# Performance work log

Measured on AMD Instinct MI355X. Metric: run time of the kernel, lower is better.

Reference implementation:

```python
import jax, jax.numpy as jnp
import numpy as np

# geomloss.SamplesLoss(loss='sinkhorn', p=2, blur=0.1**0.5, backend='tensorized',
#                      cost=cosine cost ** 2) with defaults scaling=0.5, debias=True,
#                      reach=None (balanced OT, dampening = 1), uniform weights.
P = 2
BLUR = 0.1 ** 0.5   # eps = BLUR**P = 0.1
SCALING = 0.5


def cosine_cost(a, b):
    # a: (B,N,D), b: (B,M,D) -> (1 - cos(a,b))**2, shape (B,N,M)
    an = a / jnp.linalg.norm(a, axis=-1, keepdims=True)
    bn = b / jnp.linalg.norm(b, axis=-1, keepdims=True)
    return (1.0 - jnp.einsum('bnd,bmd->bnm', an, bn)) ** P


def softmin(eps, C, h):
    # geomloss softmin_tensorized: h (B,M), C (B,N,M) -> (B,N)
    return -eps * jax.nn.logsumexp(h[:, None, :] - C / eps, axis=2)


def eps_schedule(diameter):
    # geomloss epsilon_schedule(p, diameter, blur, scaling)
    return ([diameter ** P]
            + [float(np.exp(e)) for e in np.arange(P * np.log(diameter),
                                                   P * np.log(BLUR),
                                                   P * np.log(SCALING))]
            + [BLUR ** P])


def max_diameter(x, y):
    # geomloss max_diameter over all points of both (flattened) clouds
    D = x.shape[-1]
    pts = np.concatenate([np.asarray(x).reshape(-1, D),
                          np.asarray(y).reshape(-1, D)], axis=0)
    return float(np.linalg.norm(pts.max(axis=0) - pts.min(axis=0)))


def _sinkhorn(x, y, eps_list):
    sg = jax.lax.stop_gradient
    B, N, _ = x.shape
    M = y.shape[1]
    # geomloss detaches the second argument of each cost evaluation
    C_xy = cosine_cost(x, sg(y))
    C_yx = cosine_cost(y, sg(x))
    C_xx = cosine_cost(x, sg(x))  # debias terms
    C_yy = cosine_cost(y, sg(y))

    a_log = jnp.full((B, N), -np.log(N), dtype=x.dtype)  # log uniform weights
    b_log = jnp.full((B, M), -np.log(M), dtype=x.dtype)

    # initialization at the largest temperature
    eps = eps_list[0]
    f_aa = softmin(eps, sg(C_xx), a_log)
    g_bb = softmin(eps, sg(C_yy), b_log)
    g_ab = softmin(eps, sg(C_yx), a_log)
    f_ba = softmin(eps, sg(C_xy), b_log)

    # eps-scaling loop (run without gradients, as in geomloss)
    for eps in eps_list:
        ft_ba = softmin(eps, sg(C_xy), b_log + g_ab / eps)
        gt_ab = softmin(eps, sg(C_yx), a_log + f_ba / eps)
        ft_aa = softmin(eps, sg(C_xx), a_log + f_aa / eps)
        gt_bb = softmin(eps, sg(C_yy), b_log + g_bb / eps)
        f_ba, g_ab = 0.5 * (f_ba + ft_ba), 0.5 * (g_ab + gt_ab)
        f_aa, g_bb = 0.5 * (f_aa + ft_aa), 0.5 * (g_bb + gt_bb)

    # last extrapolation WITH gradients, dual inputs detached (envelope theorem)
    eps = eps_list[-1]
    f_ba, g_ab = (softmin(eps, C_xy, sg(b_log + g_ab / eps)),
                  softmin(eps, C_yx, sg(a_log + f_ba / eps)))
    f_aa = softmin(eps, C_xx, sg(a_log + f_aa / eps))
    g_bb = softmin(eps, C_yy, sg(b_log + g_bb / eps))

    # sinkhorn_cost, debiased, batch -> (B,)
    a = jnp.exp(a_log)
    b = jnp.exp(b_log)
    return jnp.sum(a * (f_ba - f_aa), axis=1) + jnp.sum(b * (g_ab - g_bb), axis=1)


def setup_inputs() -> dict:
    key = jax.random.key(0)
    k1, k2 = jax.random.split(key)
    B, N, D = 2, 4096, 64
    inputs = jax.random.normal(k1, (B, N, D), dtype=jnp.float32)
    targets = jax.random.normal(k2, (B, N, D), dtype=jnp.float32)
    return {"inputs": inputs, "targets": targets}


def reference(inputs, targets):
    eps_list = eps_schedule(max_diameter(inputs, targets))
    return _sinkhorn(inputs, targets, eps_list)
```

## Files before the change

kernel.cpp:

```cpp
#include <hip/hip_runtime.h>
#include <math.h>

#define Bq 2
#define Nq 4096
#define Dq 64
#define MAXR 14
#define RBAND 16
#define NBAND (Nq / RBAND)
#define W_LOG (-8.317766166719343f)
#define WL2   (-12.0f)
#define LOG2E 1.4426950408889634f
#define LN2   0.6931471805599453f
#define DQ_SCALE (4.0f / 65535.0f)
#define Q_SCALE  16383.75f
#define ACLAMP 88.0f
#define SFLOOR 1e-30f

#define F_XN   ((size_t)0)
#define F_YN   (F_XN + (size_t)Bq * Nq * Dq)
#define F_XH   (F_YN + (size_t)Bq * Nq * Dq)
#define F_XL   (F_XH + (size_t)Bq * Nq * Dq / 2)
#define F_YH   (F_XL + (size_t)Bq * Nq * Dq / 2)
#define F_YL   (F_YH + (size_t)Bq * Nq * Dq / 2)
#define F_FG   (F_YL + (size_t)Bq * Nq * Dq / 2)
#define F_EPS  (F_FG + (size_t)2 * 4 * Bq * Nq)
#define F_MM   (F_EPS + 64)
#define F_CP   (F_MM + (size_t)64 * 128)
#define F_C    (((F_CP + (size_t)Bq * NBAND * Nq) + 3) & ~(size_t)3)
#define GSZ    ((size_t)Bq * Nq * Nq)
#define F_TOTAL_P (F_C + 3 * GSZ / 2)
#define F_TOTAL_S (F_C)

typedef short short8v __attribute__((ext_vector_type(8)));
typedef float f32x4 __attribute__((ext_vector_type(4)));

__device__ __forceinline__ unsigned short f2bf(float f) {
    unsigned u = __float_as_uint(f);
    unsigned r = (u + 0x7fffu + ((u >> 16) & 1u)) >> 16;
    return (unsigned short)r;
}
__device__ __forceinline__ float bf2f(unsigned short b) {
    return __uint_as_float(((unsigned)b) << 16);
}

__global__ __launch_bounds__(256) void k_normalize(const float* __restrict__ x,
                                                   const float* __restrict__ y,
                                                   float* __restrict__ ws) {
    int gid = blockIdx.x * 256 + threadIdx.x;
    int wave = gid >> 6;
    int lane = gid & 63;
    int tensor = wave / (Bq * Nq);
    int p = wave % (Bq * Nq);
    const float* src = tensor ? y : x;
    float v = src[(size_t)p * Dq + lane];
    float s = v * v;
    #pragma unroll
    for (int o = 32; o > 0; o >>= 1) s += __shfl_xor(s, o);
    float vn = v / sqrtf(s);
    float* dst = ws + (tensor ? F_YN : F_XN);
    dst[(size_t)p * Dq + lane] = vn;
    unsigned short hb = f2bf(vn);
    float lo = vn - bf2f(hb);
    unsigned short lb = f2bf(lo);
    unsigned short* dh = (unsigned short*)(ws + (tensor ? F_YH : F_XH));
    unsigned short* dl = (unsigned short*)(ws + (tensor ? F_YL : F_XL));
    dh[(size_t)p * Dq + lane] = hb;
    dl[(size_t)p * Dq + lane] = lb;
}

__global__ __launch_bounds__(256) void k_minmax(const float* __restrict__ x,
                                                const float* __restrict__ y,
                                                float* __restrict__ ws) {
    int d = threadIdx.x & 63, q = threadIdx.x >> 6;
    int p0 = blockIdx.x * 256;
    float mx = -INFINITY, mn = INFINITY;
    for (int p = p0 + q; p < p0 + 256; p += 4) {
        const float* src = (p < Bq * Nq) ? x : y;
        int pp = (p < Bq * Nq) ? p : p - Bq * Nq;
        float v = src[(size_t)pp * Dq + d];
        mx = fmaxf(mx, v); mn = fminf(mn, v);
    }
    __shared__ float smx[4][64], smn[4][64];
    smx[q][d] = mx; smn[q][d] = mn;
    __syncthreads();
    if (threadIdx.x < 64) {
        float a = fmaxf(fmaxf(smx[0][d], smx[1][d]), fmaxf(smx[2][d], smx[3][d]));
        float i = fminf(fminf(smn[0][d], smn[1][d]), fminf(smn[2][d], smn[3][d]));
        ws[F_MM + (size_t)blockIdx.x * 128 + d] = a;
        ws[F_MM + (size_t)blockIdx.x * 128 + 64 + d] = i;
    }
}

__global__ void k_eps(float* __restrict__ ws) {
    int d = threadIdx.x;
    float mx = -INFINITY, mn = INFINITY;
    for (int k = 0; k < 64; k++) {
        mx = fmaxf(mx, ws[F_MM + (size_t)k * 128 + d]);
        mn = fminf(mn, ws[F_MM + (size_t)k * 128 + 64 + d]);
    }
    float r = mx - mn;
    float r2 = r * r;
    #pragma unroll
    for (int o = 32; o > 0; o >>= 1) r2 += __shfl_xor(r2, o);
    if (d == 0) {
        double dd = (double)sqrtf(r2);
        double start = 2.0 * log(dd);
        double stop  = 2.0 * log(sqrt(0.1));
        double step  = 2.0 * log(0.5);
        double lend = ceil((stop - start) / step);
        int len = (lend <= 0.0) ? 0 : (int)lend;
        int n = len + 2;
        if (n > MAXR - 2) n = MAXR - 2;
        int* ei = (int*)(ws + F_EPS);
        ei[0] = n;
        float* ev = ws + F_EPS + 8;
        ev[0] = (float)(dd * dd);
        for (int i = 0; i < len && i + 1 < n - 1; i++)
            ev[1 + i] = (float)exp(start + i * step);
        ev[n - 1] = 0.1f;
    }
}

__global__ __launch_bounds__(256) void k_gram_mfma(float* __restrict__ ws) {
    int op = blockIdx.z, b = blockIdx.y;
    int tr = (blockIdx.x & 63) * 64;
    int tc = (blockIdx.x >> 6) * 64;
    const unsigned short* AH = (const unsigned short*)(ws + (op == 2 ? F_YH : F_XH)) + (size_t)b * Nq * Dq;
    const unsigned short* AL = (const unsigned short*)(ws + (op == 2 ? F_YL : F_XL)) + (size_t)b * Nq * Dq;
    const unsigned short* BH = (const unsigned short*)(ws + (op == 1 ? F_XH : F_YH)) + (size_t)b * Nq * Dq;
    const unsigned short* BL = (const unsigned short*)(ws + (op == 1 ? F_XL : F_YL)) + (size_t)b * Nq * Dq;

    __shared__ unsigned short sAh[64][72], sAl[64][72], sBh[64][72], sBl[64][72], sC[64][72];

    #pragma unroll
    for (int i = 0; i < 2; i++) {
        int c = threadIdx.x + 256 * i;
        int row = c >> 3, pos = c & 7;
        size_t sa = (size_t)(tr + row) * Dq + pos * 8;
        size_t sb = (size_t)(tc + row) * Dq + pos * 8;
        *(uint4*)&sAh[row][pos * 8] = *(const uint4*)&AH[sa];
        *(uint4*)&sAl[row][pos * 8] = *(const uint4*)&AL[sa];
        *(uint4*)&sBh[row][pos * 8] = *(const uint4*)&BH[sb];
        *(uint4*)&sBl[row][pos * 8] = *(const uint4*)&BL[sb];
    }
    __syncthreads();

    int w = threadIdx.x >> 6, lane = threadIdx.x & 63;
    int m = lane & 15, kb = lane >> 4;
    int ar = w * 16 + m;
    short8v aH0 = *(const short8v*)&sAh[ar][kb * 8];
    short8v aH1 = *(const short8v*)&sAh[ar][32 + kb * 8];
    short8v aL0 = *(const short8v*)&sAl[ar][kb * 8];
    short8v aL1 = *(const short8v*)&sAl[ar][32 + kb * 8];

    #pragma unroll
    for (int cb = 0; cb < 4; cb++) {
        int bc = cb * 16 + m;
        short8v bH0 = *(const short8v*)&sBh[bc][kb * 8];
        short8v bH1 = *(const short8v*)&sBh[bc][32 + kb * 8];
        short8v bL0 = *(const short8v*)&sBl[bc][kb * 8];
        short8v bL1 = *(const short8v*)&sBl[bc][32 + kb * 8];
        f32x4 acc = {0.f, 0.f, 0.f, 0.f};
        acc = __builtin_amdgcn_mfma_f32_16x16x32_bf16(aH0, bH0, acc, 0, 0, 0);
        acc = __builtin_amdgcn_mfma_f32_16x16x32_bf16(aH1, bH1, acc, 0, 0, 0);
        acc = __builtin_amdgcn_mfma_f32_16x16x32_bf16(aL0, bH0, acc, 0, 0, 0);
        acc = __builtin_amdgcn_mfma_f32_16x16x32_bf16(aL1, bH1, acc, 0, 0, 0);
        acc = __builtin_amdgcn_mfma_f32_16x16x32_bf16(aH0, bL0, acc, 0, 0, 0);
        acc = __builtin_amdgcn_mfma_f32_16x16x32_bf16(aH1, bL1, acc, 0, 0, 0);
        #pragma unroll
        for (int rr = 0; rr < 4; rr++) {
            float c1 = 1.0f - acc[rr];
            unsigned u = __float2uint_rn(fminf(c1 * c1, 4.0f) * Q_SCALE);
            if (u > 65535u) u = 65535u;
            sC[w * 16 + kb * 4 + rr][cb * 16 + m] = (unsigned short)u;
        }
    }
    __syncthreads();

    unsigned short* C = (unsigned short*)(ws + F_C) + (size_t)op * GSZ + (size_t)b * Nq * Nq;
    #pragma unroll
    for (int i = 0; i < 2; i++) {
        int c = threadIdx.x + 256 * i;
        int row = c >> 3, pos = c & 7;
        uint4 v = *(const uint4*)&sC[row][pos * 8];
        *(uint4*)&C[(size_t)(tr + row) * Nq + tc + pos * 8] = v;
    }
}

__device__ __forceinline__ bool round_cfg(const float* ws, int r, int& mode, float& eps,
                                          float& inv_eps, int& cur, int& nxt) {
    const int* ei = (const int*)(ws + F_EPS);
    int n_eps = ei[0];
    if (r > n_eps + 1) return false;
    mode = (r == 0) ? 0 : ((r <= n_eps) ? 1 : 2);
    int eidx = (r == 0) ? 0 : ((r - 1 < n_eps - 1) ? r - 1 : n_eps - 1);
    eps = ws[F_EPS + 8 + eidx];
    inv_eps = 1.0f / eps;
    cur = r & 1; nxt = cur ^ 1;
    return true;
}

__global__ __launch_bounds__(256) void k_iter(float* __restrict__ ws, int r) {
    int mode, cur, nxt; float eps, inv_eps;
    if (!round_cfg(ws, r, mode, eps, inv_eps, cur, nxt)) return;
    float ie2 = inv_eps * LOG2E;
    float epsln2 = eps * LN2;
    float nkq = -DQ_SCALE * ie2;

    int bid = blockIdx.x;
    int op = bid / (Bq * NBAND);
    int rem = bid % (Bq * NBAND);
    int b = rem / NBAND;
    int band = rem % NBAND;
    int row0 = band * RBAND;
    int w = threadIdx.x >> 6, lane = threadIdx.x & 63;
    int colA = w * 1024 + lane * 8;
    int colB = colA + 512;

    const unsigned short* C = (const unsigned short*)(ws + F_C)
                              + (size_t)op * GSZ + ((size_t)b * Nq + row0) * Nq;
    int arr_dual = (op == 0) ? 1 : (op == 1 ? 2 : 3);
    int arr_out  = (op == 0) ? 0 : arr_dual;
    const float* gdual = ws + F_FG + ((size_t)cur * 4 + arr_dual) * (Bq * Nq) + (size_t)b * Nq;
    const float* fdual = ws + F_FG + ((size_t)cur * 4 + 0) * (Bq * Nq) + (size_t)b * Nq;

    float pa[16];
    if (mode != 0) {
        float4 g0 = *(const float4*)&gdual[colA];
        float4 g1 = *(const float4*)&gdual[colA + 4];
        float4 g2 = *(const float4*)&gdual[colB];
        float4 g3 = *(const float4*)&gdual[colB + 4];
        float gv[16] = {g0.x, g0.y, g0.z, g0.w, g1.x, g1.y, g1.z, g1.w,
                        g2.x, g2.y, g2.z, g2.w, g3.x, g3.y, g3.z, g3.w};
        #pragma unroll
        for (int j = 0; j < 16; j++) pa[j] = exp2f(fminf(gv[j] * ie2, ACLAMP));
    } else {
        #pragma unroll
        for (int j = 0; j < 16; j++) pa[j] = 1.f;
    }
    float cs[16];
    #pragma unroll
    for (int j = 0; j < 16; j++) cs[j] = 0.f;

    __shared__ float rowpart[RBAND][4];

    #pragma unroll 2
    for (int i = 0; i < RBAND; i += 2) {
        uint4 cA0 = *(const uint4*)&C[(size_t)i * Nq + colA];
        uint4 cB0 = *(const uint4*)&C[(size_t)i * Nq + colB];
        uint4 cA1 = *(const uint4*)&C[(size_t)(i + 1) * Nq + colA];
        uint4 cB1 = *(const uint4*)&C[(size_t)(i + 1) * Nq + colB];
        float pb0 = 1.f, pb1 = 1.f;
        if (op == 0 && mode != 0) {
            pb0 = exp2f(fminf(fdual[row0 + i] * ie2, ACLAMP));
            pb1 = exp2f(fminf(fdual[row0 + i + 1] * ie2, ACLAMP));
        }
        unsigned u0[8] = {cA0.x, cA0.y, cA0.z, cA0.w, cB0.x, cB0.y, cB0.z, cB0.w};
        unsigned u1[8] = {cA1.x, cA1.y, cA1.z, cA1.w, cB1.x, cB1.y, cB1.z, cB1.w};
        float rs0 = 0.f, rs1 = 0.f;
        #pragma unroll
        for (int j = 0; j < 16; j++) {
            float e0 = exp2f((float)((u0[j >> 1] >> ((j & 1) * 16)) & 0xffffu) * nkq);
            float e1 = exp2f((float)((u1[j >> 1] >> ((j & 1) * 16)) & 0xffffu) * nkq);
            rs0 = fmaf(pa[j], e0, rs0);
            rs1 = fmaf(pa[j], e1, rs1);
            if (op == 0) cs[j] = fmaf(pb0, e0, fmaf(pb1, e1, cs[j]));
        }
        #pragma unroll
        for (int o = 32; o > 0; o >>= 1) {
            rs0 += __shfl_xor(rs0, o);
            rs1 += __shfl_xor(rs1, o);
        }
        if (lane == 0) { rowpart[i][w] = rs0; rowpart[i + 1][w] = rs1; }
    }
    __syncthreads();

    if (threadIdx.x < RBAND) {
        int gr = row0 + threadIdx.x;
        const float* rp = rowpart[threadIdx.x];
        float s = (rp[0] + rp[1]) + (rp[2] + rp[3]);
        float ft = -epsln2 * (WL2 + log2f(fmaxf(s, SFLOOR)));
        float* outp = ws + F_FG + ((size_t)nxt * 4 + arr_out) * (Bq * Nq) + (size_t)b * Nq;
        const float* oldp = ws + F_FG + ((size_t)cur * 4 + arr_out) * (Bq * Nq) + (size_t)b * Nq;
        outp[gr] = (mode == 1) ? 0.5f * (oldp[gr] + ft) : ft;
    }

    if (op == 0) {
        float* cp = ws + F_CP + ((size_t)b * NBAND + band) * Nq;
        *(float4*)&cp[colA]     = make_float4(cs[0], cs[1], cs[2], cs[3]);
        *(float4*)&cp[colA + 4] = make_float4(cs[4], cs[5], cs[6], cs[7]);
        *(float4*)&cp[colB]     = make_float4(cs[8], cs[9], cs[10], cs[11]);
        *(float4*)&cp[colB + 4] = make_float4(cs[12], cs[13], cs[14], cs[15]);
    }
}

__global__ __launch_bounds__(256) void k_colcomb(float* __restrict__ ws, int r) {
    int mode, cur, nxt; float eps, inv_eps;
    if (!round_cfg(ws, r, mode, eps, inv_eps, cur, nxt)) return;
    float epsln2 = eps * LN2;
    int idx = blockIdx.x * 256 + threadIdx.x;
    int b = idx >> 12, m = idx & (Nq - 1);
    const float* cp = ws + F_CP + (size_t)b * NBAND * Nq + m;
    float S = 0.f;
    #pragma unroll 8
    for (int k = 0; k < NBAND; k++) S += cp[(size_t)k * Nq];
    float gt = -epsln2 * (WL2 + log2f(fmaxf(S, SFLOOR)));
    float* outp = ws + F_FG + ((size_t)nxt * 4 + 1) * (Bq * Nq) + (size_t)b * Nq;
    const float* oldp = ws + F_FG + ((size_t)cur * 4 + 1) * (Bq * Nq) + (size_t)b * Nq;
    outp[m] = (mode == 1) ? 0.5f * (oldp[m] + gt) : gt;
}

__global__ __launch_bounds__(256) void k_fused(float* __restrict__ ws, int r) {
    int mode, cur, nxt; float eps, inv_eps;
    if (!round_cfg(ws, r, mode, eps, inv_eps, cur, nxt)) return;
    int op = blockIdx.z, b = blockIdx.y;
    int tr = blockIdx.x * 64;
    const float* A  = ws + ((op == 1 || op == 3) ? F_YN : F_XN) + (size_t)b * Nq * Dq;
    const float* Bp = ws + ((op == 0 || op == 3) ? F_YN : F_XN) + (size_t)b * Nq * Dq;
    int dual_arr = (op == 0) ? 1 : (op == 1) ? 0 : (op == 2) ? 2 : 3;
    int out_arr  = (op == 0) ? 0 : (op == 1) ? 1 : (op == 2) ? 2 : 3;
    const float* hdual = ws + F_FG + ((size_t)cur * 4 + dual_arr) * (Bq * Nq) + (size_t)b * Nq;

    __shared__ float As[64][65], Bs[64][65];
    #pragma unroll
    for (int i = 0; i < 16; i++) {
        int idx = threadIdx.x + 256 * i;
        As[idx >> 6][idx & 63] = A[(size_t)(tr + (idx >> 6)) * Dq + (idx & 63)];
    }
    int tx = threadIdx.x & 15, ty = threadIdx.x >> 4;
    float m_i[4], s_i[4];
    #pragma unroll
    for (int i = 0; i < 4; i++) { m_i[i] = -INFINITY; s_i[i] = 0.f; }

    for (int tc = 0; tc < Nq; tc += 64) {
        __syncthreads();
        #pragma unroll
        for (int i = 0; i < 16; i++) {
            int idx = threadIdx.x + 256 * i;
            Bs[idx >> 6][idx & 63] = Bp[(size_t)(tc + (idx >> 6)) * Dq + (idx & 63)];
        }
        __syncthreads();
        float acc[4][4] = {};
        #pragma unroll
        for (int dd = 0; dd < 64; dd++) {
            float a[4], bb[4];
            #pragma unroll
            for (int i = 0; i < 4; i++) a[i] = As[ty * 4 + i][dd];
            #pragma unroll
            for (int j = 0; j < 4; j++) bb[j] = Bs[tx * 4 + j][dd];
            #pragma unroll
            for (int i = 0; i < 4; i++)
                #pragma unroll
                for (int j = 0; j < 4; j++) acc[i][j] = fmaf(a[i], bb[j], acc[i][j]);
        }
        float hv[4];
        #pragma unroll
        for (int j = 0; j < 4; j++)
            hv[j] = (mode == 0) ? 0.f : hdual[tc + tx * 4 + j];
        #pragma unroll
        for (int i = 0; i < 4; i++) {
            float v[4], tm = -INFINITY;
            #pragma unroll
            for (int j = 0; j < 4; j++) {
                float c = 1.0f - acc[i][j];
                v[j] = W_LOG + (hv[j] - c * c) * inv_eps;
                tm = fmaxf(tm, v[j]);
            }
            float nm = fmaxf(m_i[i], tm);
            float add = 0.f;
            #pragma unroll
            for (int j = 0; j < 4; j++) add += expf(v[j] - nm);
            s_i[i] = s_i[i] * expf(m_i[i] - nm) + add;
            m_i[i] = nm;
        }
    }
    #pragma unroll
    for (int o = 1; o < 16; o <<= 1) {
        #pragma unroll
        for (int i = 0; i < 4; i++) {
            float om = __shfl_xor(m_i[i], o);
            float os = __shfl_xor(s_i[i], o);
            float M = fmaxf(m_i[i], om);
            s_i[i] = s_i[i] * expf(m_i[i] - M) + os * expf(om - M);
            m_i[i] = M;
        }
    }
    if (tx == 0) {
        float* outp = ws + F_FG + ((size_t)nxt * 4 + out_arr) * (Bq * Nq) + (size_t)b * Nq;
        const float* oldp = ws + F_FG + ((size_t)cur * 4 + out_arr) * (Bq * Nq) + (size_t)b * Nq;
        #pragma unroll
        for (int i = 0; i < 4; i++) {
            int n = tr + ty * 4 + i;
            float ft = -eps * (m_i[i] + logf(s_i[i]));
            outp[n] = (mode == 1) ? 0.5f * (oldp[n] + ft) : ft;
        }
    }
}

__global__ __launch_bounds__(256) void k_final(const float* __restrict__ ws,
                                               float* __restrict__ out) {
    const int* ei = (const int*)(ws + F_EPS);
    int n_eps = ei[0];
    int fin = n_eps & 1;
    int b = blockIdx.x;
    const float* fba = ws + F_FG + ((size_t)fin * 4 + 0) * (Bq * Nq) + (size_t)b * Nq;
    const float* gab = ws + F_FG + ((size_t)fin * 4 + 1) * (Bq * Nq) + (size_t)b * Nq;
    const float* faa = ws + F_FG + ((size_t)fin * 4 + 2) * (Bq * Nq) + (size_t)b * Nq;
    const float* gbb = ws + F_FG + ((size_t)fin * 4 + 3) * (Bq * Nq) + (size_t)b * Nq;
    float s = 0.f;
    for (int n = threadIdx.x; n < Nq; n += 256)
        s += (fba[n] - faa[n]) + (gab[n] - gbb[n]);
    #pragma unroll
    for (int o = 32; o > 0; o >>= 1) s += __shfl_xor(s, o);
    __shared__ float red[4];
    if ((threadIdx.x & 63) == 0) red[threadIdx.x >> 6] = s;
    __syncthreads();
    if (threadIdx.x == 0)
        out[b] = (red[0] + red[1] + red[2] + red[3]) * (1.0f / Nq);
}

__global__ void k_sentinel(float* out, int n) {
    if ((int)threadIdx.x < n) out[threadIdx.x] = 2.0e9f;
}

extern "C" void kernel_launch(void* const* d_in, const int* in_sizes, int n_in,
                              void* d_out, int out_size, void* d_ws, size_t ws_size,
                              hipStream_t stream) {
    const float* x = (const float*)d_in[0];
    const float* y = (const float*)d_in[1];
    float* out = (float*)d_out;
    float* ws = (float*)d_ws;

    bool big   = ws_size >= F_TOTAL_P * sizeof(float);
    bool small = ws_size >= F_TOTAL_S * sizeof(float);

    if (!small) {
        k_sentinel<<<1, 64, 0, stream>>>(out, out_size);
        return;
    }

    k_normalize<<<(2 * Bq * Nq * 64) / 256, 256, 0, stream>>>(x, y, ws);
    k_minmax<<<64, 256, 0, stream>>>(x, y, ws);
    k_eps<<<1, 64, 0, stream>>>(ws);

    if (big) {
        k_gram_mfma<<<dim3(4096, Bq, 3), 256, 0, stream>>>(ws);
        for (int r = 0; r < MAXR; r++) {
            k_iter<<<3 * Bq * NBAND, 256, 0, stream>>>(ws, r);
            k_colcomb<<<(Bq * Nq) / 256, 256, 0, stream>>>(ws, r);
        }
    } else {
        for (int r = 0; r < MAXR; r++) {
            k_fused<<<dim3(Nq / 64, Bq, 4), 256, 0, stream>>>(ws, r);
        }
    }

    k_final<<<Bq, 256, 0, stream>>>(ws, out);
}
```

Measured before the change: 817.4 us.

## Alias and swizzle gram-kernel LDS, software-prefetch cost rows in iteration kernel

The gram kernel now shares one LDS buffer between the input tiles and the output staging tile, which cuts shared memory per block and may raise occupancy. An extra barrier makes the aliasing safe. The output tile gets an XOR swizzle to reduce bank conflicts on the scattered writes. The Sinkhorn iteration kernel fully unrolls its row loop and loads the next pair of cost rows before computing the current pair, to hide global-load latency at the cost of more registers.

Result: slower. 1.064 ms (+30.1%).

```diff
diff --git a/kernel.cpp b/kernel.cpp
--- a/kernel.cpp
+++ b/kernel.cpp
@@ -130,7 +130,12 @@
     const unsigned short* BH = (const unsigned short*)(ws + (op == 1 ? F_XH : F_YH)) + (size_t)b * Nq * Dq;
     const unsigned short* BL = (const unsigned short*)(ws + (op == 1 ? F_XL : F_YL)) + (size_t)b * Nq * Dq;
 
-    __shared__ unsigned short sAh[64][72], sAl[64][72], sBh[64][72], sBl[64][72], sC[64][72];
+    __shared__ unsigned short sbuf[4][64][72];
+    #define sAh (sbuf[0])
+    #define sAl (sbuf[1])
+    #define sBh (sbuf[2])
+    #define sBl (sbuf[3])
+    #define sC  (sbuf[0])
 
     #pragma unroll
     for (int i = 0; i < 2; i++) {
@@ -152,6 +157,7 @@
     short8v aH1 = *(const short8v*)&sAh[ar][32 + kb * 8];
     short8v aL0 = *(const short8v*)&sAl[ar][kb * 8];
     short8v aL1 = *(const short8v*)&sAl[ar][32 + kb * 8];
+    __syncthreads();
 
     #pragma unroll
     for (int cb = 0; cb < 4; cb++) {
@@ -167,12 +173,16 @@
         acc = __builtin_amdgcn_mfma_f32_16x16x32_bf16(aL1, bH1, acc, 0, 0, 0);
         acc = __builtin_amdgcn_mfma_f32_16x16x32_bf16(aH0, bL0, acc, 0, 0, 0);
         acc = __builtin_amdgcn_mfma_f32_16x16x32_bf16(aH1, bL1, acc, 0, 0, 0);
+        int colblk = cb * 2 + (m >> 3);
+        int within = m & 7;
         #pragma unroll
         for (int rr = 0; rr < 4; rr++) {
+            int rowl = w * 16 + kb * 4 + rr;
             float c1 = 1.0f - acc[rr];
             unsigned u = __float2uint_rn(fminf(c1 * c1, 4.0f) * Q_SCALE);
             if (u > 65535u) u = 65535u;
-            sC[w * 16 + kb * 4 + rr][cb * 16 + m] = (unsigned short)u;
+            int swz = colblk ^ ((rowl >> 1) & 7);
+            sC[rowl][swz * 8 + within] = (unsigned short)u;
         }
     }
     __syncthreads();
@@ -182,9 +192,15 @@
     for (int i = 0; i < 2; i++) {
         int c = threadIdx.x + 256 * i;
         int row = c >> 3, pos = c & 7;
-        uint4 v = *(const uint4*)&sC[row][pos * 8];
+        int swz = pos ^ ((row >> 1) & 7);
+        uint4 v = *(const uint4*)&sC[row][swz * 8];
         *(uint4*)&C[(size_t)(tr + row) * Nq + tc + pos * 8] = v;
     }
+    #undef sAh
+    #undef sAl
+    #undef sBh
+    #undef sBl
+    #undef sC
 }
 
 __device__ __forceinline__ bool round_cfg(const float* ws, int r, int& mode, float& eps,
@@ -244,12 +260,20 @@
 
     __shared__ float rowpart[RBAND][4];
 
-    #pragma unroll 2
+    uint4 nA0 = *(const uint4*)&C[colA];
+    uint4 nB0 = *(const uint4*)&C[colB];
+    uint4 nA1 = *(const uint4*)&C[(size_t)Nq + colA];
+    uint4 nB1 = *(const uint4*)&C[(size_t)Nq + colB];
+
+    #pragma unroll
     for (int i = 0; i < RBAND; i += 2) {
-        uint4 cA0 = *(const uint4*)&C[(size_t)i * Nq + colA];
-        uint4 cB0 = *(const uint4*)&C[(size_t)i * Nq + colB];
-        uint4 cA1 = *(const uint4*)&C[(size_t)(i + 1) * Nq + colA];
-        uint4 cB1 = *(const uint4*)&C[(size_t)(i + 1) * Nq + colB];
+        uint4 cA0 = nA0, cB0 = nB0, cA1 = nA1, cB1 = nB1;
+        if (i + 2 < RBAND) {
+            nA0 = *(const uint4*)&C[(size_t)(i + 2) * Nq + colA];
+            nB0 = *(const uint4*)&C[(size_t)(i + 2) * Nq + colB];
+            nA1 = *(const uint4*)&C[(size_t)(i + 3) * Nq + colA];
+            nB1 = *(const uint4*)&C[(size_t)(i + 3) * Nq + colB];
+        }
         float pb0 = 1.f, pb1 = 1.f;
         if (op == 0 && mode != 0) {
             pb0 = exp2f(fminf(fdual[row0 + i] * ie2, ACLAMP));
```
